# Kernel optimization log

Hardware: AMD Instinct MI355X
Metric: run time of the kernel (lower is better)

## Reference

```python
import jax, jax.numpy as jnp
import numpy as np

EMBED_DIM = 768
NUM_HEADS = 12
KEY_DIM = EMBED_DIM // NUM_HEADS
B, S = 2, 2048

def _xavier(key, shape):
    # xavier_uniform over last-two dims (fan_in = shape[-2], fan_out = shape[-1])
    fan_in, fan_out = shape[-2], shape[-1]
    limit = jnp.sqrt(6.0 / (fan_in + fan_out)).astype(jnp.float32)
    return jax.random.uniform(key, shape, jnp.float32, -limit, limit)

def setup_inputs() -> dict:
    key = jax.random.key(0)
    kq, kk, kv, kwq, kwk, kwv, kw, km = jax.random.split(key, 8)
    q = jax.random.normal(kq, (B, S, EMBED_DIM), jnp.float32)
    k = jax.random.normal(kk, (B, S, EMBED_DIM), jnp.float32)
    v = jax.random.normal(kv, (B, S, EMBED_DIM), jnp.float32)
    # per-head projection weights stacked: [H, E, Dk]
    Wq = _xavier(kwq, (NUM_HEADS, EMBED_DIM, KEY_DIM))
    Wk = _xavier(kwk, (NUM_HEADS, EMBED_DIM, KEY_DIM))
    Wv = _xavier(kwv, (NUM_HEADS, EMBED_DIM, KEY_DIM))
    W = _xavier(kw, (EMBED_DIM, EMBED_DIM))
    mask = jax.random.randint(km, (B, 1, S, S), 0, 2).astype(jnp.int32)
    return {"q": q, "k": k, "v": v, "mask": mask, "Wq": Wq, "Wk": Wk, "Wv": Wv, "W": W}

def reference(q, k, v, mask, Wq, Wk, Wv, W):
    scale = 1.0 / jnp.sqrt(jnp.asarray(KEY_DIM, q.dtype))
    Q = jnp.einsum('bse,hed->bhsd', q, Wq)  # [B,H,S,Dk]
    K = jnp.einsum('bse,hed->bhsd', k, Wk)
    V = jnp.einsum('bse,hed->bhsd', v, Wv)
    Z = jnp.einsum('bhsd,bhtd->bhst', Q, K) * scale  # [B,H,S,S]
    Z = jnp.where(mask == 0, jnp.asarray(-1e9, Z.dtype), Z)
    score = jax.nn.softmax(Z, axis=-1)
    out = jnp.einsum('bhst,bhtd->bhsd', score, V)  # [B,H,S,Dk]
    # concat heads along last dim (head order = list order)
    concat = out.transpose(0, 2, 1, 3).reshape(q.shape[0], q.shape[1], EMBED_DIM)
    return concat @ W
```

## Files before the change

kernel.cpp:

```cpp
#include <hip/hip_runtime.h>
#include <stdint.h>

typedef uint16_t u16;
typedef __attribute__((ext_vector_type(8))) short bf16x8;
typedef __attribute__((ext_vector_type(4))) float f32x4;
typedef __attribute__((ext_vector_type(16))) float f32x16;

#define EMB 768
#define NH 12
#define DK 64
#define BB 2
#define SS 2048
#define SCL 0.1803368801111244f
#define M0  24.0f

__device__ __forceinline__ u16 f2bf(float x) {
  union { float f; uint32_t u; } v; v.f = x;
  uint32_t r = v.u + 0x7fffu + ((v.u >> 16) & 1u);
  return (u16)(r >> 16);
}

__device__ __forceinline__ uint32_t pk2(float a, float b) {
  uint32_t d;
  asm("v_cvt_pk_bf16_f32 %0, %1, %2" : "=v"(d) : "v"(a), "v"(b));
  return d;
}

__device__ __forceinline__ void gld16(const u16* g, u16* l) {
  __builtin_amdgcn_global_load_lds((const __attribute__((address_space(1))) void*)g,
                                   (__attribute__((address_space(3))) void*)l, 16, 0, 0);
}

__global__ void pack_all(const float* __restrict__ wq, const float* __restrict__ wk,
                         const float* __restrict__ wv, const float* __restrict__ w,
                         const int* __restrict__ mask,
                         u16* __restrict__ wqkvT, u16* __restrict__ wT,
                         uint64_t* __restrict__ bits) {
  uint32_t tl = blockIdx.x * 256 + threadIdx.x;
  const uint32_t WTOT = 4u * EMB * EMB;
  if (tl < WTOT) {
    int z = tl / (EMB * EMB);
    int t = tl - z * (EMB * EMB);
    int n = t / EMB, e = t - n * EMB;
    if (z < 3) {
      const float* src = z == 0 ? wq : (z == 1 ? wk : wv);
      float vv = src[((n >> 6) * EMB + e) * DK + (n & 63)];
      if (z == 0) vv *= SCL;
      wqkvT[(size_t)z * EMB * EMB + t] = f2bf(vv);
    } else {
      wT[t] = f2bf(w[e * EMB + n]);
    }
  } else {
    uint32_t widx = tl - WTOT;
    uint32_t wv64 = widx >> 6;
    uint32_t lane = widx & 63;
    uint32_t b  = wv64 >> 12;
    uint32_t qg = (wv64 >> 6) & 63;
    uint32_t tg = wv64 & 63;
    uint32_t c = lane & 31, hi = lane >> 5;
    const int* mp = mask + (((size_t)b * 2048 + qg * 32 + c) * 2048 + tg * 32 + hi * 4);
    int4 q0 = *(const int4*)mp;
    int4 q1 = *(const int4*)(mp + 8);
    int4 q2 = *(const int4*)(mp + 16);
    int4 q3 = *(const int4*)(mp + 24);
    uint64_t* wout = bits + (size_t)wv64 * 16;
    unsigned long long ball;
#define BAL(u, arr)                                                   \
    ball = __ballot(arr.x != 0); if (lane == 0) wout[u * 4 + 0] = ball; \
    ball = __ballot(arr.y != 0); if (lane == 0) wout[u * 4 + 1] = ball; \
    ball = __ballot(arr.z != 0); if (lane == 0) wout[u * 4 + 2] = ball; \
    ball = __ballot(arr.w != 0); if (lane == 0) wout[u * 4 + 3] = ball;
    BAL(0, q0) BAL(1, q1) BAL(2, q2) BAL(3, q3)
#undef BAL
  }
}

#define GEMM_MFMA_BODY64(Ab, Bb)                                                \
    bf16x8 af[2], bfr[4];                                                       \
    _Pragma("unroll")                                                           \
    for (int i = 0; i < 2; ++i)                                                 \
      af[i] = *(const bf16x8*)((Ab) + (wr * 32 + i * 16 + c) * 32 + quad * 8);  \
    _Pragma("unroll")                                                           \
    for (int j = 0; j < 4; ++j)                                                 \
      bfr[j] = *(const bf16x8*)((Bb) + (wc * 64 + j * 16 + c) * 32 + quad * 8); \
    _Pragma("unroll")                                                           \
    for (int i = 0; i < 2; ++i)                                                 \
      _Pragma("unroll")                                                         \
      for (int j = 0; j < 4; ++j)                                               \
        acc[i][j] = __builtin_amdgcn_mfma_f32_16x16x32_bf16(af[i], bfr[j], acc[i][j], 0, 0, 0);

__device__ __forceinline__ void gemm_f32A_pipe64(const float* __restrict__ A,
                                                 const u16* __restrict__ Bt, int Kdim,
                                                 int m0, int n0, u16* As, u16* Bs,
                                                 f32x4 (&acc)[2][4]) {
  const int tid = threadIdx.x;
  const int lane = tid & 63, quad = lane >> 4, c = lane & 15;
  const int wr = (tid >> 6) >> 1, wc = (tid >> 6) & 1;
  const int arow = tid >> 2, acol = (tid & 3) * 8;
  float4 a0, a1;
#define LOAD_A(kk)                                                     \
  {                                                                    \
    const float* src = A + (size_t)(m0 + arow) * Kdim + (kk) + acol;   \
    a0 = *(const float4*)src; a1 = *(const float4*)(src + 4);          \
  }
#define ISSUE_B(kk, buf)                                               \
  _Pragma("unroll")                                                    \
  for (int r = 0; r < 2; ++r) {                                        \
    int bo = r * 4096 + tid * 16;                                      \
    gld16(Bt + (size_t)(n0 + (bo >> 6)) * Kdim + (kk) + ((bo & 63) >> 1), \
          Bs + (buf) * 4096 + (bo >> 1));                              \
  }
  LOAD_A(0); ISSUE_B(0, 0);
  for (int kk = 0; kk < Kdim; kk += 32) {
    const int buf = (kk >> 5) & 1;
    {
      uint4 pkv = { pk2(a0.x, a0.y), pk2(a0.z, a0.w),
                    pk2(a1.x, a1.y), pk2(a1.z, a1.w) };
      *(uint4*)(As + buf * 2048 + arow * 32 + acol) = pkv;
    }
    __syncthreads();
    if (kk + 32 < Kdim) { LOAD_A(kk + 32); ISSUE_B(kk + 32, buf ^ 1); }
    const u16* Ab = As + buf * 2048;
    const u16* Bb = Bs + buf * 4096;
    GEMM_MFMA_BODY64(Ab, Bb)
  }
#undef LOAD_A
#undef ISSUE_B
}

__device__ __forceinline__ void gemm_bf16A_pipe64(const u16* __restrict__ A,
                                                  const u16* __restrict__ Bt, int Kdim,
                                                  int m0, int n0, u16* As, u16* Bs,
                                                  f32x4 (&acc)[2][4]) {
  const int tid = threadIdx.x;
  const int lane = tid & 63, quad = lane >> 4, c = lane & 15;
  const int wr = (tid >> 6) >> 1, wc = (tid >> 6) & 1;
#define ISSUE_AB(kk, buf)                                              \
  {                                                                    \
    gld16(A + (size_t)(m0 + (tid >> 2)) * Kdim + (kk) + (tid & 3) * 8, \
          As + (buf) * 2048 + tid * 8);                                \
    _Pragma("unroll")                                                  \
    for (int r = 0; r < 2; ++r) {                                      \
      int bo = r * 4096 + tid * 16;                                    \
      gld16(Bt + (size_t)(n0 + (bo >> 6)) * Kdim + (kk) + ((bo & 63) >> 1), \
            Bs + (buf) * 4096 + (bo >> 1));                            \
    }                                                                  \
  }
  ISSUE_AB(0, 0);
  for (int kk = 0; kk < Kdim; kk += 32) {
    const int buf = (kk >> 5) & 1;
    __syncthreads();
    if (kk + 32 < Kdim) { ISSUE_AB(kk + 32, buf ^ 1); }
    const u16* Ab = As + buf * 2048;
    const u16* Bb = Bs + buf * 4096;
    GEMM_MFMA_BODY64(Ab, Bb)
  }
#undef ISSUE_AB
}

__launch_bounds__(256, 4)
__global__ void gemm_qkv(const float* __restrict__ q, const float* __restrict__ k,
                         const float* __restrict__ v, const u16* __restrict__ wt3,
                         u16* __restrict__ Qp, u16* __restrict__ Kp, u16* __restrict__ Vt) {
  __shared__ u16 As[2 * 64 * 32];
  __shared__ u16 Bs[2 * 128 * 32];
  const int id = blockIdx.x;
  const int xcd = id & 7, s = id >> 3;
  const int panel = xcd * 24 + s / 6;
  const int ntile = s - (s / 6) * 6;
  const int z = panel >> 6, mt = panel & 63;
  const int m0 = mt * 64, n0 = ntile * 128;
  const float* A = z == 0 ? q : (z == 1 ? k : v);
  const u16* Bt = wt3 + (size_t)z * EMB * EMB;
  f32x4 acc[2][4];
  const f32x4 fz = {0.f, 0.f, 0.f, 0.f};
#pragma unroll
  for (int i = 0; i < 2; ++i)
#pragma unroll
    for (int j = 0; j < 4; ++j) acc[i][j] = fz;
  gemm_f32A_pipe64(A, Bt, EMB, m0, n0, As, Bs, acc);
  const int tid = threadIdx.x, lane = tid & 63, quad = lane >> 4, c = lane & 15;
  const int wr = (tid >> 6) >> 1, wc = (tid >> 6) & 1;
  if (z < 2) {
    u16* C = z == 0 ? Qp : Kp;
#pragma unroll
    for (int i = 0; i < 2; ++i)
#pragma unroll
      for (int j = 0; j < 4; ++j) {
        int row = m0 + wr * 32 + i * 16 + quad * 4;
        int col = n0 + wc * 64 + j * 16 + c;
#pragma unroll
        for (int r = 0; r < 4; r += 2) {
          uint32_t d = pk2(acc[i][j][r], acc[i][j][r + 1]);
          C[(size_t)(row + r) * EMB + col] = (u16)d;
          C[(size_t)(row + r + 1) * EMB + col] = (u16)(d >> 16);
        }
      }
  } else {
#pragma unroll
    for (int i = 0; i < 2; ++i)
#pragma unroll
      for (int j = 0; j < 4; ++j) {
        int row = m0 + wr * 32 + i * 16 + quad * 4;
        int col = n0 + wc * 64 + j * 16 + c;
        int b = row >> 11, ss = row & 2047;
        int h = col >> 6, d = col & 63;
        uint2 pk = { pk2(acc[i][j][0], acc[i][j][1]), pk2(acc[i][j][2], acc[i][j][3]) };
        *(uint2*)(Vt + ((size_t)(b * NH + h) * DK + d) * SS + ss) = pk;
      }
  }
}

__launch_bounds__(256, 4)
__global__ void gemm_out(const u16* __restrict__ A, const u16* __restrict__ Bt,
                         float* __restrict__ C) {
  __shared__ u16 As[2 * 64 * 32];
  __shared__ u16 Bs[2 * 128 * 32];
  const int id = blockIdx.x;
  const int xcd = id & 7, s = id >> 3;
  const int panel = xcd * 8 + s / 6;
  const int ntile = s - (s / 6) * 6;
  const int m0 = panel * 64, n0 = ntile * 128;
  f32x4 acc[2][4];
  const f32x4 fz = {0.f, 0.f, 0.f, 0.f};
#pragma unroll
  for (int i = 0; i < 2; ++i)
#pragma unroll
    for (int j = 0; j < 4; ++j) acc[i][j] = fz;
  gemm_bf16A_pipe64(A, Bt, EMB, m0, n0, As, Bs, acc);
  const int tid = threadIdx.x, lane = tid & 63, quad = lane >> 4, c = lane & 15;
  const int wr = (tid >> 6) >> 1, wc = (tid >> 6) & 1;
#pragma unroll
  for (int i = 0; i < 2; ++i)
#pragma unroll
    for (int j = 0; j < 4; ++j)
#pragma unroll
      for (int r = 0; r < 4; ++r) {
        int row = m0 + wr * 32 + i * 16 + quad * 4 + r;
        int col = n0 + wc * 64 + j * 16 + c;
        C[(size_t)row * EMB + col] = acc[i][j][r];
      }
}

__launch_bounds__(512, 4)
__global__ void attn(const u16* __restrict__ Qp, const u16* __restrict__ Kp,
                     const u16* __restrict__ Vt, const uint64_t* __restrict__ MW,
                     u16* __restrict__ AO) {
  __shared__ __align__(16) u16 sm[2 * 128 * 72 + 2 * 64 * 136];
  u16* Ks0 = sm;
  u16* Vs0 = sm + 2 * 128 * 72;

  const int tid = threadIdx.x, lane = tid & 63;
  const int c = lane & 31, hi = lane >> 5;
  const int w = tid >> 6;
  const int wq2 = w >> 2, th = w & 3;

  const int wid = blockIdx.x;
  const int xcd = wid & 7, slot = wid >> 3;
  const int bh = xcd + 8 * (slot >> 5);
  const int mtile = slot & 31;
  const int b = bh / NH, h = bh - b * NH;
  const int m0 = mtile * 64;

  const size_t qkbase = (size_t)b * SS * EMB + (size_t)h * DK;
  const size_t vtbase = (size_t)bh * DK * SS;

  bf16x8 aq[4];
  {
    const u16* qr = Qp + qkbase + (size_t)(m0 + wq2 * 32 + c) * EMB + hi * 8;
    aq[0] = *(const bf16x8*)(qr);
    aq[1] = *(const bf16x8*)(qr + 16);
    aq[2] = *(const bf16x8*)(qr + 32);
    aq[3] = *(const bf16x8*)(qr + 48);
  }

  const int srK = tid >> 2, scK = (tid & 3) * 16;
  const int srV = tid >> 3, scV = (tid & 7) * 16;
  const u16* gK = Kp + qkbase + (size_t)srK * EMB + scK;
  const u16* gV = Vt + vtbase + (size_t)srV * SS + scV;
  bf16x8 kr0, kr1, vr0, vr1;
#define LOADKV(t0) {                                             \
    const u16* gk_ = gK + (size_t)(t0) * EMB;                    \
    kr0 = *(const bf16x8*)gk_; kr1 = *(const bf16x8*)(gk_ + 8);  \
    const u16* gv_ = gV + (t0);                                  \
    vr0 = *(const bf16x8*)gv_; vr1 = *(const bf16x8*)(gv_ + 8); }
#define STOREKV(buf) {                                           \
    u16* ks_ = Ks0 + (buf) * (128 * 72) + srK * 72 + scK;        \
    *(bf16x8*)ks_ = kr0; *(bf16x8*)(ks_ + 8) = kr1;              \
    u16* vs_ = Vs0 + (buf) * (64 * 136) + srV * 136 + scV;       \
    *(bf16x8*)vs_ = vr0; *(bf16x8*)(vs_ + 8) = vr1; }

  const int thu = __builtin_amdgcn_readfirstlane(th);
  const int qgu = __builtin_amdgcn_readfirstlane(mtile * 2 + wq2);
  const uint64_t* mwb = MW + (((size_t)b * 64 + qgu) * 64) * 16 + thu * 16;
#define LOADMSK(m, it) {                                         \
    const uint64_t* mp_ = mwb + (size_t)(it) * 64;               \
    _Pragma("unroll")                                            \
    for (int r_ = 0; r_ < 16; ++r_) m[r_] = mp_[r_]; }

  float fNEG = -1e9f, fM0 = -M0;
  float lr = 0.f;
  f32x16 o0, o1;
#pragma unroll
  for (int r_ = 0; r_ < 16; ++r_) { o0[r_] = 0.f; o1[r_] = 0.f; }

  uint64_t mA[16], mB[16];
  LOADKV(0); LOADMSK(mA, 0);

#define BODY(it, buf, mc, mn) {                                                   \
    STOREKV(buf);                                                                 \
    __syncthreads();                                                              \
    if ((it) < 15) { LOADKV(((it) + 1) * 128); LOADMSK(mn, (it) + 1); }           \
     \
    f32x16 s;                                                                     \
    _Pragma("unroll")                                                             \
    for (int r_ = 0; r_ < 16; ++r_) {                                             \
      float t_;                                                                   \
      asm("v_cndmask_b32 %0, %1, %2, %3"                                          \
          : "=v"(t_) : "v"(fNEG), "v"(fM0), "s"(mc[r_]));                         \
      s[r_] = t_;                                                                 \
    }                                                                             \
                                          \
    const u16* kb_ = Ks0 + (buf) * (128 * 72) + (th * 32 + c) * 72 + hi * 8;      \
    _Pragma("unroll")                                                             \
    for (int ks_ = 0; ks_ < 4; ++ks_) {                                           \
      bf16x8 kf_ = *(const bf16x8*)(kb_ + ks_ * 16);                              \
      s = __builtin_amdgcn_mfma_f32_32x32x16_bf16(kf_, aq[ks_], s, 0, 0, 0);      \
    }                                                                             \
                               \
    _Pragma("unroll")                                                             \
    for (int r_ = 0; r_ < 16; ++r_) s[r_] = __builtin_amdgcn_exp2f(s[r_]);        \
    lr += ((s[0] + s[1]) + (s[2] + s[3])) + ((s[4] + s[5]) + (s[6] + s[7]))       \
        + ((s[8] + s[9]) + (s[10] + s[11])) + ((s[12] + s[13]) + (s[14] + s[15]));\
                      \
    uint32_t x0 = pk2(s[0], s[1]),  x1 = pk2(s[2], s[3]);                         \
    uint32_t y0 = pk2(s[4], s[5]),  y1 = pk2(s[6], s[7]);                         \
    uint32_t z0 = pk2(s[8], s[9]),  z1 = pk2(s[10], s[11]);                       \
    uint32_t w0 = pk2(s[12], s[13]), w1 = pk2(s[14], s[15]);                      \
    asm("v_permlane32_swap_b32 %0, %1" : "+v"(x0), "+v"(y0));                     \
    asm("v_permlane32_swap_b32 %0, %1" : "+v"(x1), "+v"(y1));                     \
    asm("v_permlane32_swap_b32 %0, %1" : "+v"(z0), "+v"(w0));                     \
    asm("v_permlane32_swap_b32 %0, %1" : "+v"(z1), "+v"(w1));                     \
    bf16x8 pa0, pa1;                                                              \
    { union { uint32_t u[4]; bf16x8 v; } cv;                                      \
      cv.u[0] = x0; cv.u[1] = x1; cv.u[2] = y0; cv.u[3] = y1; pa0 = cv.v;         \
      cv.u[0] = z0; cv.u[1] = z1; cv.u[2] = w0; cv.u[3] = w1; pa1 = cv.v; }       \
                                  \
    const u16* vb_ = Vs0 + (buf) * (64 * 136) + c * 136 + th * 32 + hi * 8;       \
    {                                                                             \
      bf16x8 vf_;                                                                 \
      vf_ = *(const bf16x8*)(vb_);                                                \
      o0 = __builtin_amdgcn_mfma_f32_32x32x16_bf16(vf_, pa0, o0, 0, 0, 0);        \
      vf_ = *(const bf16x8*)(vb_ + 16);                                           \
      o0 = __builtin_amdgcn_mfma_f32_32x32x16_bf16(vf_, pa1, o0, 0, 0, 0);        \
      vf_ = *(const bf16x8*)(vb_ + 32 * 136);                                     \
      o1 = __builtin_amdgcn_mfma_f32_32x32x16_bf16(vf_, pa0, o1, 0, 0, 0);        \
      vf_ = *(const bf16x8*)(vb_ + 32 * 136 + 16);                                \
      o1 = __builtin_amdgcn_mfma_f32_32x32x16_bf16(vf_, pa1, o1, 0, 0, 0);        \
    } }

  for (int i2 = 0; i2 < 8; ++i2) {
    BODY(i2 * 2,     0, mA, mB)
    BODY(i2 * 2 + 1, 1, mB, mA)
  }
#undef BODY
#undef LOADKV
#undef STOREKV
#undef LOADMSK

  lr += __shfl_xor(lr, 32);
  __syncthreads();
  float* Of = (float*)sm;
  float* Lf = (float*)sm + 4 * 64 * 65;
  {
    int row = wq2 * 32 + c;
#pragma unroll
    for (int r_ = 0; r_ < 16; ++r_) {
      int d = (r_ & 3) + 8 * (r_ >> 2) + 4 * hi;
      Of[(th * 64 + row) * 65 + d]      = o0[r_];
      Of[(th * 64 + row) * 65 + 32 + d] = o1[r_];
    }
    if (hi == 0) Lf[row * 4 + th] = lr;
  }
  __syncthreads();
  {
    int qrow = tid >> 3, d0 = (tid & 7) * 8;
    float lt = Lf[qrow * 4 + 0] + Lf[qrow * 4 + 1] + Lf[qrow * 4 + 2] + Lf[qrow * 4 + 3];
    float inv = 1.f / fmaxf(lt, 1e-20f);
    float acc[8];
#pragma unroll
    for (int e = 0; e < 8; ++e) acc[e] = 0.f;
#pragma unroll
    for (int t_ = 0; t_ < 4; ++t_)
#pragma unroll
      for (int e = 0; e < 8; ++e) acc[e] += Of[(t_ * 64 + qrow) * 65 + d0 + e];
    uint32_t dw[4];
#pragma unroll
    for (int e = 0; e < 4; ++e) dw[e] = pk2(acc[2 * e] * inv, acc[2 * e + 1] * inv);
    *(uint4*)(AO + qkbase + (size_t)(m0 + qrow) * EMB + d0) = *(uint4*)dw;
  }
}

extern "C" void kernel_launch(void* const* d_in, const int* in_sizes, int n_in,
                              void* d_out, int out_size, void* d_ws, size_t ws_size,
                              hipStream_t stream) {
  const float* q  = (const float*)d_in[0];
  const float* k  = (const float*)d_in[1];
  const float* v  = (const float*)d_in[2];
  const int* mask = (const int*)d_in[3];
  const float* Wq = (const float*)d_in[4];
  const float* Wk = (const float*)d_in[5];
  const float* Wv = (const float*)d_in[6];
  const float* W  = (const float*)d_in[7];
  float* out = (float*)d_out;

  u16* Kp = (u16*)d_out;
  u16* Vt = (u16*)d_out + 3145728;

  u16* ws    = (u16*)d_ws;
  u16* Qp    = ws;
  u16* WqkvT = ws + 3145728;
  u16* WT    = ws + 3145728 + 1769472;
  uint64_t* mb64 = (uint64_t*)(ws + 5505024);
  u16* AO = Qp;

  pack_all<<<dim3(11264), 256, 0, stream>>>(Wq, Wk, Wv, W, mask, WqkvT, WT, mb64);
  gemm_qkv<<<dim3(1152), 256, 0, stream>>>(q, k, v, WqkvT, Qp, Kp, Vt);
  attn<<<dim3(768), 512, 0, stream>>>(Qp, Kp, Vt, mb64, AO);
  gemm_out<<<dim3(384), 256, 0, stream>>>(AO, WT, out);
}
```

Before: 226.9 us.

## Use 4-slot LDS ring with prefetch distance two in projection GEMMs

```diff
diff --git a/kernel.cpp b/kernel.cpp
--- a/kernel.cpp
+++ b/kernel.cpp
@@ -13,6 +13,10 @@
 #define SS 2048
 #define SCL 0.1803368801111244f
 #define M0  24.0f
+
+#define WAITV(n)  asm volatile("s_waitcnt vmcnt(" #n ")" ::: "memory")
+#define WAITVL(n) asm volatile("s_waitcnt vmcnt(" #n ") lgkmcnt(0)" ::: "memory")
+#define FENCE()   asm volatile("" ::: "memory")
 
 __device__ __forceinline__ u16 f2bf(float x) {
   union { float f; uint32_t u; } v; v.f = x;
@@ -89,10 +93,10 @@
       for (int j = 0; j < 4; ++j)                                               \
         acc[i][j] = __builtin_amdgcn_mfma_f32_16x16x32_bf16(af[i], bfr[j], acc[i][j], 0, 0, 0);
 
-__device__ __forceinline__ void gemm_f32A_pipe64(const float* __restrict__ A,
-                                                 const u16* __restrict__ Bt, int Kdim,
-                                                 int m0, int n0, u16* As, u16* Bs,
-                                                 f32x4 (&acc)[2][4]) {
+__device__ __forceinline__ void gemm_f32A_ring(const float* __restrict__ A,
+                                               const u16* __restrict__ Bt,
+                                               int m0, int n0, u16* As, u16* Bs,
+                                               f32x4 (&acc)[2][4]) {
   const int tid = threadIdx.x;
   const int lane = tid & 63, quad = lane >> 4, c = lane & 15;
   const int wr = (tid >> 6) >> 1, wc = (tid >> 6) & 1;
@@ -100,70 +104,80 @@
   float4 a0, a1;
 #define LOAD_A(kk)                                                     \
   {                                                                    \
-    const float* src = A + (size_t)(m0 + arow) * Kdim + (kk) + acol;   \
+    const float* src = A + (size_t)(m0 + arow) * EMB + (kk) + acol;    \
     a0 = *(const float4*)src; a1 = *(const float4*)(src + 4);          \
   }
-#define ISSUE_B(kk, buf)                                               \
+#define WRITE_A(r4)                                                    \
+  {                                                                    \
+    uint4 pkv = { pk2(a0.x, a0.y), pk2(a0.z, a0.w),                    \
+                  pk2(a1.x, a1.y), pk2(a1.z, a1.w) };                  \
+    *(uint4*)(As + (r4) * 2048 + arow * 32 + acol) = pkv;              \
+  }
+#define ISSUE_B(kk, r4)                                                \
   _Pragma("unroll")                                                    \
   for (int r = 0; r < 2; ++r) {                                        \
     int bo = r * 4096 + tid * 16;                                      \
-    gld16(Bt + (size_t)(n0 + (bo >> 6)) * Kdim + (kk) + ((bo & 63) >> 1), \
-          Bs + (buf) * 4096 + (bo >> 1));                              \
+    gld16(Bt + (size_t)(n0 + (bo >> 6)) * EMB + (kk) + ((bo & 63) >> 1), \
+          Bs + (r4) * 4096 + (bo >> 1));                               \
   }
   LOAD_A(0); ISSUE_B(0, 0);
-  for (int kk = 0; kk < Kdim; kk += 32) {
-    const int buf = (kk >> 5) & 1;
-    {
-      uint4 pkv = { pk2(a0.x, a0.y), pk2(a0.z, a0.w),
-                    pk2(a1.x, a1.y), pk2(a1.z, a1.w) };
-      *(uint4*)(As + buf * 2048 + arow * 32 + acol) = pkv;
-    }
-    __syncthreads();
-    if (kk + 32 < Kdim) { LOAD_A(kk + 32); ISSUE_B(kk + 32, buf ^ 1); }
-    const u16* Ab = As + buf * 2048;
-    const u16* Bb = Bs + buf * 4096;
+  WRITE_A(0);
+  LOAD_A(32); ISSUE_B(32, 1);
+#pragma unroll 4
+  for (int t = 0; t < 24; ++t) {
+    if (t + 1 < 24) WRITE_A((t + 1) & 3);
+    if (t + 1 < 24) { WAITVL(2); } else { WAITVL(0); }
+    __builtin_amdgcn_s_barrier();
+    FENCE();
+    if (t + 2 < 24) { LOAD_A(t * 32 + 64); ISSUE_B(t * 32 + 64, (t + 2) & 3); }
+    const u16* Ab = As + (t & 3) * 2048;
+    const u16* Bb = Bs + (t & 3) * 4096;
     GEMM_MFMA_BODY64(Ab, Bb)
   }
 #undef LOAD_A
+#undef WRITE_A
 #undef ISSUE_B
 }
 
-__device__ __forceinline__ void gemm_bf16A_pipe64(const u16* __restrict__ A,
-                                                  const u16* __restrict__ Bt, int Kdim,
-                                                  int m0, int n0, u16* As, u16* Bs,
-                                                  f32x4 (&acc)[2][4]) {
+__device__ __forceinline__ void gemm_bf16A_ring(const u16* __restrict__ A,
+                                                const u16* __restrict__ Bt,
+                                                int m0, int n0, u16* As, u16* Bs,
+                                                f32x4 (&acc)[2][4]) {
   const int tid = threadIdx.x;
   const int lane = tid & 63, quad = lane >> 4, c = lane & 15;
   const int wr = (tid >> 6) >> 1, wc = (tid >> 6) & 1;
-#define ISSUE_AB(kk, buf)                                              \
+#define ISSUE_AB(kk, r4)                                               \
   {                                                                    \
-    gld16(A + (size_t)(m0 + (tid >> 2)) * Kdim + (kk) + (tid & 3) * 8, \
-          As + (buf) * 2048 + tid * 8);                                \
+    gld16(A + (size_t)(m0 + (tid >> 2)) * EMB + (kk) + (tid & 3) * 8,  \
+          As + (r4) * 2048 + tid * 8);                                 \
     _Pragma("unroll")                                                  \
     for (int r = 0; r < 2; ++r) {                                      \
       int bo = r * 4096 + tid * 16;                                    \
-      gld16(Bt + (size_t)(n0 + (bo >> 6)) * Kdim + (kk) + ((bo & 63) >> 1), \
-            Bs + (buf) * 4096 + (bo >> 1));                            \
+      gld16(Bt + (size_t)(n0 + (bo >> 6)) * EMB + (kk) + ((bo & 63) >> 1), \
+            Bs + (r4) * 4096 + (bo >> 1));                             \
     }                                                                  \
   }
   ISSUE_AB(0, 0);
-  for (int kk = 0; kk < Kdim; kk += 32) {
-    const int buf = (kk >> 5) & 1;
-    __syncthreads();
-    if (kk + 32 < Kdim) { ISSUE_AB(kk + 32, buf ^ 1); }
-    const u16* Ab = As + buf * 2048;
-    const u16* Bb = Bs + buf * 4096;
+  ISSUE_AB(32, 1);
+#pragma unroll 4
+  for (int t = 0; t < 24; ++t) {
+    if (t + 1 < 24) { WAITV(3); } else { WAITV(0); }
+    __builtin_amdgcn_s_barrier();
+    FENCE();
+    if (t + 2 < 24) { ISSUE_AB(t * 32 + 64, (t + 2) & 3); }
+    const u16* Ab = As + (t & 3) * 2048;
+    const u16* Bb = Bs + (t & 3) * 4096;
     GEMM_MFMA_BODY64(Ab, Bb)
   }
 #undef ISSUE_AB
 }
 
-__launch_bounds__(256, 4)
+__launch_bounds__(256, 3)
 __global__ void gemm_qkv(const float* __restrict__ q, const float* __restrict__ k,
                          const float* __restrict__ v, const u16* __restrict__ wt3,
                          u16* __restrict__ Qp, u16* __restrict__ Kp, u16* __restrict__ Vt) {
-  __shared__ u16 As[2 * 64 * 32];
-  __shared__ u16 Bs[2 * 128 * 32];
+  __shared__ __align__(16) u16 As[4 * 64 * 32];
+  __shared__ __align__(16) u16 Bs[4 * 128 * 32];
   const int id = blockIdx.x;
   const int xcd = id & 7, s = id >> 3;
   const int panel = xcd * 24 + s / 6;
@@ -178,7 +192,7 @@
   for (int i = 0; i < 2; ++i)
 #pragma unroll
     for (int j = 0; j < 4; ++j) acc[i][j] = fz;
-  gemm_f32A_pipe64(A, Bt, EMB, m0, n0, As, Bs, acc);
+  gemm_f32A_ring(A, Bt, m0, n0, As, Bs, acc);
   const int tid = threadIdx.x, lane = tid & 63, quad = lane >> 4, c = lane & 15;
   const int wr = (tid >> 6) >> 1, wc = (tid >> 6) & 1;
   if (z < 2) {
@@ -211,11 +225,11 @@
   }
 }
 
-__launch_bounds__(256, 4)
+__launch_bounds__(256, 3)
 __global__ void gemm_out(const u16* __restrict__ A, const u16* __restrict__ Bt,
                          float* __restrict__ C) {
-  __shared__ u16 As[2 * 64 * 32];
-  __shared__ u16 Bs[2 * 128 * 32];
+  __shared__ __align__(16) u16 As[4 * 64 * 32];
+  __shared__ __align__(16) u16 Bs[4 * 128 * 32];
   const int id = blockIdx.x;
   const int xcd = id & 7, s = id >> 3;
   const int panel = xcd * 8 + s / 6;
@@ -227,7 +241,7 @@
   for (int i = 0; i < 2; ++i)
 #pragma unroll
     for (int j = 0; j < 4; ++j) acc[i][j] = fz;
-  gemm_bf16A_pipe64(A, Bt, EMB, m0, n0, As, Bs, acc);
+  gemm_bf16A_ring(A, Bt, m0, n0, As, Bs, acc);
   const int tid = threadIdx.x, lane = tid & 63, quad = lane >> 4, c = lane & 15;
   const int wr = (tid >> 6) >> 1, wc = (tid >> 6) & 1;
 #pragma unroll
```

New measurement: 231.5 us. 1.02x slower.
